# Kernel tuning notes

Hardware: AMD Instinct MI355X
Metric: run time of the kernel (lower is better)

Reference implementation:

```python
import jax, jax.numpy as jnp
import numpy as np
import math

EMBED_DIM = 128
NUM_HEADS = 8
HDIM = EMBED_DIM // NUM_HEADS


def setup_inputs() -> dict:
    key = jax.random.key(0)
    kq, kh, km, k1, k2, k3, k4 = jax.random.split(key, 7)
    B, NQ, GS = 32, 1024, 1024
    q = jax.random.normal(kq, (B, NQ, EMBED_DIM), dtype=jnp.float32)
    h = jax.random.normal(kh, (B, GS, EMBED_DIM), dtype=jnp.float32)
    mask = jax.random.bernoulli(km, 0.15, (B, NQ, GS))
    stdv = 1.0 / math.sqrt(HDIM)
    Wq = jax.random.uniform(k1, (NUM_HEADS, EMBED_DIM, HDIM), jnp.float32, -stdv, stdv)
    Wk = jax.random.uniform(k2, (NUM_HEADS, EMBED_DIM, HDIM), jnp.float32, -stdv, stdv)
    Wv = jax.random.uniform(k3, (NUM_HEADS, EMBED_DIM, HDIM), jnp.float32, -stdv, stdv)
    stdv_o = 1.0 / math.sqrt(EMBED_DIM)
    Wout = jax.random.uniform(k4, (NUM_HEADS, HDIM, EMBED_DIM), jnp.float32, -stdv_o, stdv_o)
    return {"q": q, "h": h, "mask": mask, "Wq": Wq, "Wk": Wk, "Wv": Wv, "Wout": Wout}


def reference(q, h, mask, Wq, Wk, Wv, Wout):
    norm = 1.0 / math.sqrt(HDIM)
    # per-head projections: [h, b, n, e]
    Q = jnp.einsum('bnd,hde->hbne', q, Wq)
    K = jnp.einsum('bgd,hde->hbge', h, Wk)
    V = jnp.einsum('bgd,hde->hbge', h, Wv)
    compat = norm * jnp.einsum('hbne,hbge->hbng', Q, K)  # [h,b,nq,gs]
    m = mask[None]  # broadcast over heads
    compat = jnp.where(m, -jnp.inf, compat)
    attn = jax.nn.softmax(compat, axis=-1)
    attn = jnp.where(m, 0.0, attn)
    heads = jnp.einsum('hbng,hbge->hbne', attn, V)
    out = jnp.einsum('hbne,hed->bnd', heads, Wout)
    return out
```

## Files before the change

### kernel.cpp

```cpp
#include <hip/hip_runtime.h>

typedef unsigned short u16;
typedef unsigned int   u32;
typedef short bf16x8 __attribute__((ext_vector_type(8)));
typedef float f32x2  __attribute__((ext_vector_type(2)));
typedef float f32x4  __attribute__((ext_vector_type(4)));
typedef float f32x16 __attribute__((ext_vector_type(16)));

#define NB  32
#define NQ  1024
#define GS  1024
#define NH  8
#define SCQ (0.25f * 1.4426950408889634f)
#define MBIG (-1.0e30f)

#define MFMA16(a, b, c) __builtin_amdgcn_mfma_f32_16x16x32_bf16(a, b, c, 0, 0, 0)
#define MFMA32(a, b, c) __builtin_amdgcn_mfma_f32_32x32x16_bf16(a, b, c, 0, 0, 0)

__device__ __forceinline__ u16 f2bf(float f) {
    u32 u = __float_as_uint(f);
    return (u16)((u + 0x7fffu + ((u >> 16) & 1u)) >> 16);
}
__device__ __forceinline__ u32 pk2bf(float a, float b) {
    u32 ua = __float_as_uint(a) + 0x8000u;
    u32 ub = __float_as_uint(b) + 0x8000u;
    return __builtin_amdgcn_perm(ub, ua, 0x07060302u);
}

__global__ __launch_bounds__(256) void wprep(const float* __restrict__ Wq,
                                             const float* __restrict__ Wk,
                                             const float* __restrict__ Wv,
                                             const float* __restrict__ Wout,
                                             u16* __restrict__ Wp) {
    int g = blockIdx.x * 256 + threadIdx.x;
    int m = g >> 14;
    int i = g & 16383;
    const float* src = (m == 0) ? Wq : (m == 1) ? Wk : (m == 2) ? Wv : Wout;
    float sc = (m == 0) ? SCQ : 1.0f;
    float v;
    if (m < 3) { int cc = i >> 7, k = i & 127;  v = src[(cc >> 4) * 2048 + k * 16 + (cc & 15)]; }
    else       { int d  = i >> 7, he = i & 127; v = src[(he >> 4) * 2048 + (he & 15) * 128 + d]; }
    Wp[m * 16384 + i] = f2bf(v * sc);
}

template <int MODE>
__device__ __forceinline__ void mgemm(const float* __restrict__ Ain,
                                      const u16* __restrict__ Wpm,
                                      u16* __restrict__ outb,
                                      u16* As, u16* Ws, int row0) {
    const int t    = threadIdx.x;
    const int wv   = t >> 6;
    const int lane = t & 63;
    const int quad = lane >> 4;
    const int c    = lane & 15;

#pragma unroll
    for (int g0 = 0; g0 < 2048; g0 += 256) {
        int g = g0 + t;
        int row = g >> 4, k0 = (g & 15) * 8;
        const float4* ap = (const float4*)&Ain[(size_t)(row0 + row) * 128 + k0];
        float4 a0 = ap[0], a1 = ap[1];
        int4 pk;
        pk.x = (int)pk2bf(a0.x, a0.y);
        pk.y = (int)pk2bf(a0.z, a0.w);
        pk.z = (int)pk2bf(a1.x, a1.y);
        pk.w = (int)pk2bf(a1.z, a1.w);
        *(int4*)&As[row * 136 + k0] = pk;
    }
#pragma unroll
    for (int g0 = 0; g0 < 2048; g0 += 256) {
        int g = g0 + t;
        int cc = g >> 4, k0 = (g & 15) * 8;
        *(int4*)&Ws[cc * 136 + k0] = *(const int4*)&Wpm[cc * 128 + k0];
    }
    __syncthreads();

    const f32x4 zf = {0.f, 0.f, 0.f, 0.f};
    f32x4 acc[2][8];
#pragma unroll
    for (int s = 0; s < 2; ++s)
#pragma unroll
        for (int j = 0; j < 8; ++j) acc[s][j] = zf;

#pragma unroll
    for (int kt = 0; kt < 4; ++kt) {
        bf16x8 af0 = *(const bf16x8*)&As[(wv * 32 + c) * 136 + kt * 32 + quad * 8];
        bf16x8 af1 = *(const bf16x8*)&As[(wv * 32 + 16 + c) * 136 + kt * 32 + quad * 8];
#pragma unroll
        for (int j = 0; j < 8; ++j) {
            bf16x8 bfr = *(const bf16x8*)&Ws[(j * 16 + c) * 136 + kt * 32 + quad * 8];
            acc[0][j] = MFMA16(af0, bfr, acc[0][j]);
            acc[1][j] = MFMA16(af1, bfr, acc[1][j]);
        }
    }

    __syncthreads();
    u16* Os = As;
#pragma unroll
    for (int s = 0; s < 2; ++s)
#pragma unroll
        for (int j = 0; j < 8; ++j)
#pragma unroll
            for (int r = 0; r < 4; ++r) {
                int lrow = wv * 32 + s * 16 + quad * 4 + r;
                int col  = j * 16 + c;
                u16 v = f2bf(acc[s][j][r]);
                if (MODE == 0) {
                    Os[lrow * 136 + col] = v;
                } else {
                    Os[col * 136 + lrow] = v;
                }
            }
    __syncthreads();

    if (MODE == 0) {
#pragma unroll
        for (int it = 0; it < 8; ++it) {
            int chunk = it * 256 + t;
            int lrow = chunk >> 4, c0 = (chunk & 15) * 8;
            *(int4*)&outb[(size_t)(row0 + lrow) * 128 + c0] =
                *(const int4*)&Os[lrow * 136 + c0];
        }
    } else {
        int bI = row0 >> 10, tb0 = row0 & 1023;
#pragma unroll
        for (int it = 0; it < 8; ++it) {
            int chunk = it * 256 + t;
            int col = chunk >> 4, t0 = (chunk & 15) * 8;
            *(int4*)&outb[(size_t)bI * (128 * 1024) + (size_t)col * 1024 + tb0 + t0] =
                *(const int4*)&Os[col * 136 + t0];
        }
    }
}

__global__ __launch_bounds__(256, 2) void proj_mfma(const float* __restrict__ q,
                                                    const float* __restrict__ h,
                                                    const u16* __restrict__ Wp,
                                                    u16* __restrict__ Qb,
                                                    u16* __restrict__ Kb,
                                                    u16* __restrict__ Vtg) {
    __shared__ u16 As[128 * 136];
    __shared__ u16 Ws[128 * 136];
    int row0 = blockIdx.x * 128;
    if (blockIdx.y == 0)      mgemm<0>(q, Wp,         Qb,  As, Ws, row0);
    else if (blockIdx.y == 1) mgemm<0>(h, Wp + 16384, Kb,  As, Ws, row0);
    else                      mgemm<2>(h, Wp + 32768, Vtg, As, Ws, row0);
}

__global__ __launch_bounds__(512, 4) void flash_mfma(const u16* __restrict__ Qb,
                                                     const u16* __restrict__ Kb,
                                                     const u16* __restrict__ Vtg,
                                                     const int* __restrict__ mask,
                                                     const u16* __restrict__ Wob,
                                                     float* __restrict__ out) {
    __shared__ u16 Kt[32 * 136];
    __shared__ u16 Vtt[128 * 36];
    __shared__ u16 Ps[NH][32 * 36];
    __shared__ float Mf[32 * 36];

    const int b    = blockIdx.x;
    const int q0   = blockIdx.y * 32;
    const int t    = threadIdx.x;
    const int hh   = t >> 6;
    const int lane = t & 63;
    const int quad = lane >> 4;
    const int c    = lane & 15;
    const int qq   = lane & 31;
    const int hi   = lane >> 5;

    const f32x4 zf = {0.f, 0.f, 0.f, 0.f};

    bf16x8 qf = *(const bf16x8*)&Qb[((size_t)b * NQ + q0 + qq) * 128 +
                                    hh * 16 + hi * 8];

    f32x4 O[2] = {zf, zf};
    float lsum = 0.f;

    const int skey = t >> 4;
    const int sd0  = (t & 15) * 8;
    const int vdim = t >> 2;
    const int vs0  = (t & 3) * 8;
    const int mrow = t >> 4;
    const int mk0  = (t & 15) * 2;

    const u16* Kptr = &Kb[((size_t)b * GS + skey) * 128 + sd0];
    const u16* Vptr = &Vtg[(size_t)b * (128 * 1024) + (size_t)vdim * 1024 + vs0];
    const int* Mptr = &mask[((size_t)b * NQ + q0 + mrow) * GS + mk0];

    int4 kreg = *(const int4*)Kptr;
    int4 vreg = *(const int4*)Vptr;
    int2 mreg = *(const int2*)Mptr;

    for (int g0 = 0; g0 < GS; g0 += 32) {
        __syncthreads();
        *(int4*)&Kt[skey * 136 + sd0] = kreg;
        *(int4*)&Vtt[vdim * 36 + vs0] = vreg;
        f32x2 mm;
        mm.x = mreg.x ? MBIG : 0.f;
        mm.y = mreg.y ? MBIG : 0.f;
        *(f32x2*)&Mf[mrow * 36 + mk0] = mm;
        __syncthreads();

        if (g0 + 32 < GS) {
            Kptr += 32 * 128;  kreg = *(const int4*)Kptr;
            Vptr += 32;        vreg = *(const int4*)Vptr;
            Mptr += 32;        mreg = *(const int2*)Mptr;
        }

        bf16x8 kf = *(const bf16x8*)&Kt[qq * 136 + hh * 16 + hi * 8];
        f32x16 c0;
#pragma unroll
        for (int blk = 0; blk < 4; ++blk) {
            f32x4 m = *(const f32x4*)&Mf[qq * 36 + 8 * blk + 4 * hi];
            c0[4 * blk + 0] = m.x;
            c0[4 * blk + 1] = m.y;
            c0[4 * blk + 2] = m.z;
            c0[4 * blk + 3] = m.w;
        }
        f32x16 sc = MFMA32(kf, qf, c0);

        bf16x8 vf = *(const bf16x8*)&Vtt[(hh * 16 + c) * 36 + quad * 8];

        float e[16];
#pragma unroll
        for (int r = 0; r < 16; ++r) e[r] = __builtin_amdgcn_exp2f(sc[r]);
        lsum += ((e[0] + e[1]) + (e[2] + e[3])) + ((e[4] + e[5]) + (e[6] + e[7])) +
                (((e[8] + e[9]) + (e[10] + e[11])) + ((e[12] + e[13]) + (e[14] + e[15])));
#pragma unroll
        for (int blk = 0; blk < 4; ++blk) {
            int2 pw;
            pw.x = (int)pk2bf(e[4 * blk + 0], e[4 * blk + 1]);
            pw.y = (int)pk2bf(e[4 * blk + 2], e[4 * blk + 3]);
            *(int2*)&Ps[hh][qq * 36 + 8 * blk + 4 * hi] = pw;
        }

#pragma unroll
        for (int s = 0; s < 2; ++s) {
            bf16x8 pf = *(const bf16x8*)&Ps[hh][(s * 16 + c) * 36 + quad * 8];
            O[s] = MFMA16(pf, vf, O[s]);
        }
    }

    lsum += __shfl_xor(lsum, 32);
    float rlv = (lsum > 0.f) ? 1.f / lsum : 0.f;

    __syncthreads();
    u16* Hs = Kt;
#pragma unroll
    for (int s = 0; s < 2; ++s)
#pragma unroll
        for (int r = 0; r < 4; ++r) {
            float rlq = __shfl(rlv, s * 16 + quad * 4 + r);
            Hs[(s * 16 + quad * 4 + r) * 136 + hh * 16 + c] =
                f2bf(O[s][r] * rlq);
        }
    __syncthreads();

    f32x4 oacc[2] = {zf, zf};
#pragma unroll
    for (int kt = 0; kt < 4; ++kt) {
        bf16x8 bfr = *(const bf16x8*)&Wob[(hh * 16 + c) * 128 + kt * 32 + quad * 8];
#pragma unroll
        for (int s = 0; s < 2; ++s) {
            bf16x8 af = *(const bf16x8*)&Hs[(s * 16 + c) * 136 + kt * 32 + quad * 8];
            oacc[s] = MFMA16(af, bfr, oacc[s]);
        }
    }
#pragma unroll
    for (int s = 0; s < 2; ++s)
#pragma unroll
        for (int r = 0; r < 4; ++r)
            out[((size_t)b * NQ + q0 + s * 16 + quad * 4 + r) * 128 + hh * 16 + c] =
                oacc[s][r];
}

extern "C" void kernel_launch(void* const* d_in, const int* in_sizes, int n_in,
                              void* d_out, int out_size, void* d_ws, size_t ws_size,
                              hipStream_t stream) {
    const float* q    = (const float*)d_in[0];
    const float* h    = (const float*)d_in[1];
    const int*   mask = (const int*)d_in[2];
    const float* Wq   = (const float*)d_in[3];
    const float* Wk   = (const float*)d_in[4];
    const float* Wv   = (const float*)d_in[5];
    const float* Wout = (const float*)d_in[6];
    float* out = (float*)d_out;

    const size_t NTOK = (size_t)NB * NQ;
    u16* Qb  = (u16*)d_ws;
    u16* Kb  = Qb + NTOK * 128;
    u16* Vtg = Kb + NTOK * 128;
    u16* Wp  = Vtg + NTOK * 128;

    wprep<<<dim3(256), 256, 0, stream>>>(Wq, Wk, Wv, Wout, Wp);
    proj_mfma<<<dim3(256, 3), 256, 0, stream>>>(q, h, Wp, Qb, Kb, Vtg);
    flash_mfma<<<dim3(NB, NQ / 32), 512, 0, stream>>>(Qb, Kb, Vtg, mask,
                                                      Wp + 49152, out);
}
```

Before: 306.7 us.

## Restructure flash kernel to register-resident K/V, bitmask mask, and fused weight prep

The attention kernel now reads each block's full mask rows once up front, packs them into 64-bit ballot bitmasks in shared memory, and rebuilds the -inf bias from bits. K and V fragments come straight from global memory into registers, prefetched 64 keys ahead, so the per-tile shared-memory staging and the two barriers per iteration are gone. P stays in registers and feeds 32x32 MFMAs for PV without an LDS round trip. Weight conversion moves into the projection kernel, removing one launch, and the V-transpose store gains an LDS swizzle. In exchange, all K/V reads are redundant per-wave global loads with more register pressure, and each block stalls on the full mask read before its loop starts.

```diff
diff --git a/kernel.cpp b/kernel.cpp
--- a/kernel.cpp
+++ b/kernel.cpp
@@ -2,8 +2,8 @@
 
 typedef unsigned short u16;
 typedef unsigned int   u32;
+typedef unsigned long long u64;
 typedef short bf16x8 __attribute__((ext_vector_type(8)));
-typedef float f32x2  __attribute__((ext_vector_type(2)));
 typedef float f32x4  __attribute__((ext_vector_type(4)));
 typedef float f32x16 __attribute__((ext_vector_type(16)));
 
@@ -27,25 +27,10 @@
     return __builtin_amdgcn_perm(ub, ua, 0x07060302u);
 }
 
-__global__ __launch_bounds__(256) void wprep(const float* __restrict__ Wq,
-                                             const float* __restrict__ Wk,
-                                             const float* __restrict__ Wv,
-                                             const float* __restrict__ Wout,
-                                             u16* __restrict__ Wp) {
-    int g = blockIdx.x * 256 + threadIdx.x;
-    int m = g >> 14;
-    int i = g & 16383;
-    const float* src = (m == 0) ? Wq : (m == 1) ? Wk : (m == 2) ? Wv : Wout;
-    float sc = (m == 0) ? SCQ : 1.0f;
-    float v;
-    if (m < 3) { int cc = i >> 7, k = i & 127;  v = src[(cc >> 4) * 2048 + k * 16 + (cc & 15)]; }
-    else       { int d  = i >> 7, he = i & 127; v = src[(he >> 4) * 2048 + (he & 15) * 128 + d]; }
-    Wp[m * 16384 + i] = f2bf(v * sc);
-}
-
 template <int MODE>
 __device__ __forceinline__ void mgemm(const float* __restrict__ Ain,
-                                      const u16* __restrict__ Wpm,
+                                      const float* __restrict__ Wraw,
+                                      float wsc,
                                       u16* __restrict__ outb,
                                       u16* As, u16* Ws, int row0) {
     const int t    = threadIdx.x;
@@ -69,9 +54,20 @@
     }
 #pragma unroll
     for (int g0 = 0; g0 < 2048; g0 += 256) {
-        int g = g0 + t;
-        int cc = g >> 4, k0 = (g & 15) * 8;
-        *(int4*)&Ws[cc * 136 + k0] = *(const int4*)&Wpm[cc * 128 + k0];
+        int idx  = g0 + t;
+        int hk   = idx >> 1, half = idx & 1;
+        int k    = hk & 127;
+        int col0 = (hk >> 7) * 16 + half * 8;
+        const float4* wp = (const float4*)&Wraw[hk * 16 + half * 8];
+        float4 w0 = wp[0], w1 = wp[1];
+        Ws[(col0 + 0) * 136 + k] = f2bf(w0.x * wsc);
+        Ws[(col0 + 1) * 136 + k] = f2bf(w0.y * wsc);
+        Ws[(col0 + 2) * 136 + k] = f2bf(w0.z * wsc);
+        Ws[(col0 + 3) * 136 + k] = f2bf(w0.w * wsc);
+        Ws[(col0 + 4) * 136 + k] = f2bf(w1.x * wsc);
+        Ws[(col0 + 5) * 136 + k] = f2bf(w1.y * wsc);
+        Ws[(col0 + 6) * 136 + k] = f2bf(w1.z * wsc);
+        Ws[(col0 + 7) * 136 + k] = f2bf(w1.w * wsc);
     }
     __syncthreads();
 
@@ -108,7 +104,10 @@
                 if (MODE == 0) {
                     Os[lrow * 136 + col] = v;
                 } else {
-                    Os[col * 136 + lrow] = v;
+                    int u   = lrow & 15;
+                    int sw  = ((u >> 2) ^ (u >> 3)) & 1;
+                    int tbp = lrow ^ (sw ? 12 : 0);
+                    Os[col * 136 + tbp] = v;
                 }
             }
     __syncthreads();
@@ -135,16 +134,29 @@
 
 __global__ __launch_bounds__(256, 2) void proj_mfma(const float* __restrict__ q,
                                                     const float* __restrict__ h,
-                                                    const u16* __restrict__ Wp,
+                                                    const float* __restrict__ Wq,
+                                                    const float* __restrict__ Wk,
+                                                    const float* __restrict__ Wv,
+                                                    const float* __restrict__ Wout,
                                                     u16* __restrict__ Qb,
                                                     u16* __restrict__ Kb,
-                                                    u16* __restrict__ Vtg) {
+                                                    u16* __restrict__ Vtg,
+                                                    u16* __restrict__ Wob) {
     __shared__ u16 As[128 * 136];
     __shared__ u16 Ws[128 * 136];
+    int y = blockIdx.y;
+    if (y == 3) {
+        if (blockIdx.x < 64) {
+            int i = blockIdx.x * 256 + threadIdx.x;
+            int d = i >> 7, he = i & 127;
+            Wob[i] = f2bf(Wout[(he >> 4) * 2048 + (he & 15) * 128 + d]);
+        }
+        return;
+    }
     int row0 = blockIdx.x * 128;
-    if (blockIdx.y == 0)      mgemm<0>(q, Wp,         Qb,  As, Ws, row0);
-    else if (blockIdx.y == 1) mgemm<0>(h, Wp + 16384, Kb,  As, Ws, row0);
-    else                      mgemm<2>(h, Wp + 32768, Vtg, As, Ws, row0);
+    if (y == 0)      mgemm<0>(q, Wq, SCQ,  Qb,  As, Ws, row0);
+    else if (y == 1) mgemm<0>(h, Wk, 1.0f, Kb,  As, Ws, row0);
+    else             mgemm<2>(h, Wv, 1.0f, Vtg, As, Ws, row0);
 }
 
 __global__ __launch_bounds__(512, 4) void flash_mfma(const u16* __restrict__ Qb,
@@ -153,10 +165,8 @@
                                                      const int* __restrict__ mask,
                                                      const u16* __restrict__ Wob,
                                                      float* __restrict__ out) {
-    __shared__ u16 Kt[32 * 136];
-    __shared__ u16 Vtt[128 * 36];
-    __shared__ u16 Ps[NH][32 * 36];
-    __shared__ float Mf[32 * 36];
+    __shared__ u64 Mb[32][17];
+    __shared__ u16 Hs[32 * 136];
 
     const int b    = blockIdx.x;
     const int q0   = blockIdx.y * 32;
@@ -168,94 +178,120 @@
     const int qq   = lane & 31;
     const int hi   = lane >> 5;
 
-    const f32x4 zf = {0.f, 0.f, 0.f, 0.f};
+#pragma unroll
+    for (int rr = 0; rr < 4; ++rr) {
+        int row = hh * 4 + rr;
+        const int* mp = &mask[((size_t)b * NQ + q0 + row) * GS + lane];
+#pragma unroll
+        for (int jj = 0; jj < 16; ++jj) {
+            u64 bal = __ballot(mp[jj * 64] != 0);
+            if (lane == 0) Mb[row][jj] = bal;
+        }
+    }
 
     bf16x8 qf = *(const bf16x8*)&Qb[((size_t)b * NQ + q0 + qq) * 128 +
                                     hh * 16 + hi * 8];
 
-    f32x4 O[2] = {zf, zf};
+    const u16* Kp = &Kb[((size_t)b * GS + qq) * 128 + hh * 16 + hi * 8];
+    const u16* Vp = &Vtg[(size_t)b * (128 * 1024) + (size_t)(hh * 16 + c) * 1024 +
+                         hi * 8];
+
+    bf16x8 kc0 = *(const bf16x8*)(Kp);
+    bf16x8 kc1 = *(const bf16x8*)(Kp + 32 * 128);
+    bf16x8 vc0 = *(const bf16x8*)(Vp);
+    bf16x8 vc1 = *(const bf16x8*)(Vp + 16);
+    bf16x8 vc2 = *(const bf16x8*)(Vp + 32);
+    bf16x8 vc3 = *(const bf16x8*)(Vp + 48);
+
+    f32x16 O32;
+#pragma unroll
+    for (int r = 0; r < 16; ++r) O32[r] = 0.f;
     float lsum = 0.f;
-
-    const int skey = t >> 4;
-    const int sd0  = (t & 15) * 8;
-    const int vdim = t >> 2;
-    const int vs0  = (t & 3) * 8;
-    const int mrow = t >> 4;
-    const int mk0  = (t & 15) * 2;
-
-    const u16* Kptr = &Kb[((size_t)b * GS + skey) * 128 + sd0];
-    const u16* Vptr = &Vtg[(size_t)b * (128 * 1024) + (size_t)vdim * 1024 + vs0];
-    const int* Mptr = &mask[((size_t)b * NQ + q0 + mrow) * GS + mk0];
-
-    int4 kreg = *(const int4*)Kptr;
-    int4 vreg = *(const int4*)Vptr;
-    int2 mreg = *(const int2*)Mptr;
-
-    for (int g0 = 0; g0 < GS; g0 += 32) {
-        __syncthreads();
-        *(int4*)&Kt[skey * 136 + sd0] = kreg;
-        *(int4*)&Vtt[vdim * 36 + vs0] = vreg;
-        f32x2 mm;
-        mm.x = mreg.x ? MBIG : 0.f;
-        mm.y = mreg.y ? MBIG : 0.f;
-        *(f32x2*)&Mf[mrow * 36 + mk0] = mm;
-        __syncthreads();
-
-        if (g0 + 32 < GS) {
-            Kptr += 32 * 128;  kreg = *(const int4*)Kptr;
-            Vptr += 32;        vreg = *(const int4*)Vptr;
-            Mptr += 32;        mreg = *(const int2*)Mptr;
-        }
-
-        bf16x8 kf = *(const bf16x8*)&Kt[qq * 136 + hh * 16 + hi * 8];
-        f32x16 c0;
-#pragma unroll
-        for (int blk = 0; blk < 4; ++blk) {
-            f32x4 m = *(const f32x4*)&Mf[qq * 36 + 8 * blk + 4 * hi];
-            c0[4 * blk + 0] = m.x;
-            c0[4 * blk + 1] = m.y;
-            c0[4 * blk + 2] = m.z;
-            c0[4 * blk + 3] = m.w;
-        }
-        f32x16 sc = MFMA32(kf, qf, c0);
-
-        bf16x8 vf = *(const bf16x8*)&Vtt[(hh * 16 + c) * 36 + quad * 8];
-
-        float e[16];
-#pragma unroll
-        for (int r = 0; r < 16; ++r) e[r] = __builtin_amdgcn_exp2f(sc[r]);
-        lsum += ((e[0] + e[1]) + (e[2] + e[3])) + ((e[4] + e[5]) + (e[6] + e[7])) +
-                (((e[8] + e[9]) + (e[10] + e[11])) + ((e[12] + e[13]) + (e[14] + e[15])));
-#pragma unroll
-        for (int blk = 0; blk < 4; ++blk) {
-            int2 pw;
-            pw.x = (int)pk2bf(e[4 * blk + 0], e[4 * blk + 1]);
-            pw.y = (int)pk2bf(e[4 * blk + 2], e[4 * blk + 3]);
-            *(int2*)&Ps[hh][qq * 36 + 8 * blk + 4 * hi] = pw;
-        }
-
-#pragma unroll
-        for (int s = 0; s < 2; ++s) {
-            bf16x8 pf = *(const bf16x8*)&Ps[hh][(s * 16 + c) * 36 + quad * 8];
-            O[s] = MFMA16(pf, vf, O[s]);
-        }
+    const u32 mbb = __float_as_uint(MBIG);
+
+    __syncthreads();
+    u64 mw = Mb[qq][0];
+
+    for (int g0 = 0; g0 < GS; g0 += 64) {
+        u32 wlo = ((u32)mw) >> (4 * hi);
+        u32 whi = ((u32)(mw >> 32)) >> (4 * hi);
+        f32x16 c0, c1;
+#pragma unroll
+        for (int r = 0; r < 16; ++r) {
+            const int pos = (r & 3) + 8 * (r >> 2);
+            c0[r] = __uint_as_float(((u32)(((int)(wlo << (31 - pos))) >> 31)) & mbb);
+            c1[r] = __uint_as_float(((u32)(((int)(whi << (31 - pos))) >> 31)) & mbb);
+        }
+        f32x16 s0 = MFMA32(kc0, qf, c0);
+        f32x16 s1 = MFMA32(kc1, qf, c1);
+
+        bf16x8 kn0 = kc0, kn1 = kc1, vn0 = vc0, vn1 = vc1, vn2 = vc2, vn3 = vc3;
+        u64 mwn = mw;
+        if (g0 + 64 < GS) {
+            Kp += 64 * 128;
+            Vp += 64;
+            kn0 = *(const bf16x8*)(Kp);
+            kn1 = *(const bf16x8*)(Kp + 32 * 128);
+            vn0 = *(const bf16x8*)(Vp);
+            vn1 = *(const bf16x8*)(Vp + 16);
+            vn2 = *(const bf16x8*)(Vp + 32);
+            vn3 = *(const bf16x8*)(Vp + 48);
+            mwn = Mb[qq][(g0 >> 6) + 1];
+        }
+
+#pragma unroll
+        for (int r = 0; r < 16; ++r) s0[r] = __builtin_amdgcn_exp2f(s0[r]);
+        lsum += ((s0[0] + s0[1]) + (s0[2] + s0[3])) + ((s0[4] + s0[5]) + (s0[6] + s0[7])) +
+                (((s0[8] + s0[9]) + (s0[10] + s0[11])) + ((s0[12] + s0[13]) + (s0[14] + s0[15])));
+        {
+            int4 pa, pb;
+            pa.x = (int)pk2bf(s0[0],  s0[1]);  pa.y = (int)pk2bf(s0[2],  s0[3]);
+            pa.z = (int)pk2bf(s0[4],  s0[5]);  pa.w = (int)pk2bf(s0[6],  s0[7]);
+            pb.x = (int)pk2bf(s0[8],  s0[9]);  pb.y = (int)pk2bf(s0[10], s0[11]);
+            pb.z = (int)pk2bf(s0[12], s0[13]); pb.w = (int)pk2bf(s0[14], s0[15]);
+            bf16x8 p0, p1;
+            __builtin_memcpy(&p0, &pa, 16);
+            __builtin_memcpy(&p1, &pb, 16);
+            O32 = MFMA32(vc0, p0, O32);
+            O32 = MFMA32(vc1, p1, O32);
+        }
+
+#pragma unroll
+        for (int r = 0; r < 16; ++r) s1[r] = __builtin_amdgcn_exp2f(s1[r]);
+        lsum += ((s1[0] + s1[1]) + (s1[2] + s1[3])) + ((s1[4] + s1[5]) + (s1[6] + s1[7])) +
+                (((s1[8] + s1[9]) + (s1[10] + s1[11])) + ((s1[12] + s1[13]) + (s1[14] + s1[15])));
+        {
+            int4 pa, pb;
+            pa.x = (int)pk2bf(s1[0],  s1[1]);  pa.y = (int)pk2bf(s1[2],  s1[3]);
+            pa.z = (int)pk2bf(s1[4],  s1[5]);  pa.w = (int)pk2bf(s1[6],  s1[7]);
+            pb.x = (int)pk2bf(s1[8],  s1[9]);  pb.y = (int)pk2bf(s1[10], s1[11]);
+            pb.z = (int)pk2bf(s1[12], s1[13]); pb.w = (int)pk2bf(s1[14], s1[15]);
+            bf16x8 p2, p3;
+            __builtin_memcpy(&p2, &pa, 16);
+            __builtin_memcpy(&p3, &pb, 16);
+            O32 = MFMA32(vc2, p2, O32);
+            O32 = MFMA32(vc3, p3, O32);
+        }
+
+        kc0 = kn0; kc1 = kn1;
+        vc0 = vn0; vc1 = vn1; vc2 = vn2; vc3 = vn3;
+        mw  = mwn;
     }
 
     lsum += __shfl_xor(lsum, 32);
-    float rlv = (lsum > 0.f) ? 1.f / lsum : 0.f;
-
-    __syncthreads();
-    u16* Hs = Kt;
-#pragma unroll
-    for (int s = 0; s < 2; ++s)
-#pragma unroll
-        for (int r = 0; r < 4; ++r) {
-            float rlq = __shfl(rlv, s * 16 + quad * 4 + r);
-            Hs[(s * 16 + quad * 4 + r) * 136 + hh * 16 + c] =
-                f2bf(O[s][r] * rlq);
-        }
-    __syncthreads();
-
+    float rl = (lsum > 0.f) ? 1.f / lsum : 0.f;
+
+    u32 h0 = pk2bf(O32[0] * rl, O32[1] * rl);
+    u32 h1 = pk2bf(O32[2] * rl, O32[3] * rl);
+    u32 h2 = pk2bf(O32[4] * rl, O32[5] * rl);
+    u32 h3 = pk2bf(O32[6] * rl, O32[7] * rl);
+    int2 ha; ha.x = (int)h0; ha.y = (int)h1;
+    int2 hb; hb.x = (int)h2; hb.y = (int)h3;
+    *(int2*)&Hs[qq * 136 + hh * 16 + 4 * hi]     = ha;
+    *(int2*)&Hs[qq * 136 + hh * 16 + 8 + 4 * hi] = hb;
+    __syncthreads();
+
+    const f32x4 zf = {0.f, 0.f, 0.f, 0.f};
     f32x4 oacc[2] = {zf, zf};
 #pragma unroll
     for (int kt = 0; kt < 4; ++kt) {
@@ -290,10 +326,10 @@
     u16* Qb  = (u16*)d_ws;
     u16* Kb  = Qb + NTOK * 128;
     u16* Vtg = Kb + NTOK * 128;
-    u16* Wp  = Vtg + NTOK * 128;
-
-    wprep<<<dim3(256), 256, 0, stream>>>(Wq, Wk, Wv, Wout, Wp);
-    proj_mfma<<<dim3(256, 3), 256, 0, stream>>>(q, h, Wp, Qb, Kb, Vtg);
+    u16* Wob = Vtg + NTOK * 128;
+
+    proj_mfma<<<dim3(256, 4), 256, 0, stream>>>(q, h, Wq, Wk, Wv, Wout,
+                                                Qb, Kb, Vtg, Wob);
     flash_mfma<<<dim3(NB, NQ / 32), 512, 0, stream>>>(Qb, Kb, Vtg, mask,
-                                                      Wp + 49152, out);
-}
+                                                      Wob, out);
+}
```

Measured after the change: 405.4 us. 32.2% more time.
